# Performance work log

Measured on AMD Instinct MI355X. Metric: run time of the kernel, lower is better.

## Reference

```python
import jax, jax.numpy as jnp
import numpy as np

N, E, D_IN, D_OUT = 100000, 1600000, 64, 64


def setup_inputs() -> dict:
    key = jax.random.key(0)
    k0, k1, k2, k3 = jax.random.split(key, 4)
    x = jax.random.normal(k0, (N, D_IN), dtype=jnp.float32)
    edge_index = jax.random.randint(k1, (2, E), 0, N)  # [2, E] (src, dst)
    W = jax.random.normal(k2, (D_IN, D_OUT), dtype=jnp.float32) / np.sqrt(D_IN).astype(np.float32)
    b = jnp.zeros((D_OUT,), dtype=jnp.float32)
    causal_attention = jax.random.normal(k3, (D_OUT, D_OUT), dtype=jnp.float32)
    return {"x": x, "edge_index": edge_index, "W": W, "b": b,
            "causal_attention": causal_attention, "L": 1}


def gcn_conv(x, edge_index, W, b):
    # PyG GCNConv: x' = D^{-1/2} (A + I) D^{-1/2} (x W) + b
    n = x.shape[0]
    xw = x @ W  # [N, D_OUT]
    loops = jnp.arange(n)
    src = jnp.concatenate([edge_index[0], loops])  # [E+N]
    dst = jnp.concatenate([edge_index[1], loops])
    deg = jax.ops.segment_sum(jnp.ones_like(src, dtype=xw.dtype), dst, num_segments=n)
    dinv = jnp.where(deg > 0, jax.lax.rsqrt(deg), 0.0)
    norm = dinv[src] * dinv[dst]  # [E+N]
    agg = jax.ops.segment_sum(norm[:, None] * xw[src], dst, num_segments=n)  # [N, D_OUT]
    return agg + b


def reference(x, edge_index, W, b, causal_attention, L):
    x_conv = gcn_conv(x, edge_index, W, b)
    causal_weights = jax.nn.softmax(causal_attention, axis=1)  # row softmax
    return x_conv @ causal_weights  # [N, D_OUT]
```

## Files before the change

kernel.cpp:

```cpp
#include <hip/hip_runtime.h>
#include <hip/hip_bf16.h>


#define D 64
#define BSHIFT 7
#define BNODES 128
#define ARENA_CAP 3072
#define REBIN_CAP 8192
#define BIN_TILE 2048

__device__ __forceinline__ unsigned short f2bf(float f) {
    union { float f; unsigned int u; } c;
    c.f = f;
    unsigned int u = c.u;
    u += 0x7fffu + ((u >> 16) & 1u);
    return (unsigned short)(u >> 16);
}
__device__ __forceinline__ float bf2f(unsigned short r) {
    union { unsigned int u; float f; } c;
    c.u = ((unsigned int)r) << 16;
    return c.f;
}
__device__ __forceinline__ float bflo(unsigned int u) {
    union { unsigned int u; float f; } c;
    c.u = u << 16;
    return c.f;
}
__device__ __forceinline__ float bfhi(unsigned int u) {
    union { unsigned int u; float f; } c;
    c.u = u & 0xffff0000u;
    return c.f;
}

__global__ __launch_bounds__(256) void prep_kernel(const float* __restrict__ W,
                                                   const float* __restrict__ b,
                                                   const float* __restrict__ A,
                                                   float* __restrict__ M,
                                                   float* __restrict__ bs,
                                                   int* __restrict__ cursor, int nbuck) {
    __shared__ float S[D * D];
    int t = threadIdx.x;
    int gidx = blockIdx.x * 256 + t;
    if (gidx < nbuck) cursor[gidx] = gidx * ARENA_CAP;
    if (t < D) {
        float mx = -1e30f;
        for (int j = 0; j < D; j++) mx = fmaxf(mx, A[t * D + j]);
        float sum = 0.f;
        for (int j = 0; j < D; j++) {
            float v = __expf(A[t * D + j] - mx);
            S[t * D + j] = v;
            sum += v;
        }
        float inv = 1.f / sum;
        for (int j = 0; j < D; j++) S[t * D + j] *= inv;
    }
    __syncthreads();
    int k = blockIdx.x * 4 + (t >> 6);
    int j = t & 63;
    float acc = 0.f;
    for (int d = 0; d < D; d++) acc += W[k * D + d] * S[d * D + j];
    M[k * D + j] = acc;
    if (blockIdx.x == 0 && t < D) {
        float a2 = 0.f;
        for (int d = 0; d < D; d++) a2 += b[d] * S[d * D + t];
        bs[t] = a2;
    }
}

__global__ __launch_bounds__(256) void bin_kernel(const int* __restrict__ src,
                                                  const int* __restrict__ dst,
                                                  int* __restrict__ cursor,
                                                  int* __restrict__ binned, int E) {
    __shared__ int h[1024];
    __shared__ int pbuf[BIN_TILE];
    __shared__ unsigned short bb[BIN_TILE];
    int t = threadIdx.x;
    for (int i = t; i < 1024; i += 256) h[i] = 0;
    __syncthreads();
    int base = blockIdx.x * BIN_TILE;
    int cnt = min(E - base, BIN_TILE);
    for (int i = t; i < cnt; i += 256) {
        int s = src[base + i], d = dst[base + i];
        int bk = (d >> BSHIFT) & 1023;
        pbuf[i] = (s << BSHIFT) | (d & (BNODES - 1));
        bb[i] = (unsigned short)bk;
        atomicAdd(&h[bk], 1);
    }
    __syncthreads();
    for (int b = t; b < 1024; b += 256) {
        int c = h[b];
        if (c) h[b] = atomicAdd(&cursor[b], c);
    }
    __syncthreads();
    for (int i = t; i < cnt; i += 256) {
        int pos = atomicAdd(&h[bb[i]], 1);
        binned[pos] = pbuf[i];
    }
}

__global__ __launch_bounds__(256) void rebin_kernel(int* __restrict__ binned,
                                                    const int* __restrict__ cursor,
                                                    int* __restrict__ rowstart,
                                                    int* __restrict__ rowend,
                                                    float* __restrict__ dinv, int N) {
    __shared__ int buf[REBIN_CAP];
    __shared__ int h[BNODES];
    __shared__ int sc[BNODES];
    __shared__ int cur[BNODES];
    int t = threadIdx.x;
    int b = blockIdx.x;
    int s = b * ARENA_CAP;
    int cnt = cursor[b] - s;
    if (cnt > REBIN_CAP) cnt = REBIN_CAP;
    if (t < BNODES) h[t] = 0;
    __syncthreads();
    for (int i = t; i < cnt; i += 256) {
        int p = binned[s + i];
        buf[i] = p;
        atomicAdd(&h[p & (BNODES - 1)], 1);
    }
    __syncthreads();
    if (t < BNODES) sc[t] = h[t];
    __syncthreads();
    for (int off = 1; off < BNODES; off <<= 1) {
        int u = (t < BNODES && t >= off) ? sc[t - off] : 0;
        __syncthreads();
        if (t < BNODES) sc[t] += u;
        __syncthreads();
    }
    if (t < BNODES) {
        int ex = sc[t] - h[t];
        cur[t] = ex;
        int node = (b << BSHIFT) + t;
        if (node < N) {
            rowstart[node] = s + ex;
            rowend[node] = s + sc[t];
            dinv[node] = rsqrtf((float)(h[t] + 1));
        }
    }
    __syncthreads();
    for (int i = t; i < cnt; i += 256) {
        int p = buf[i];
        int pos = atomicAdd(&cur[p & (BNODES - 1)], 1);
        binned[s + pos] = (int)((unsigned)p >> BSHIFT);
    }
}

__global__ __launch_bounds__(256) void zmat_kernel(const float* __restrict__ x,
                                                   const float* __restrict__ M,
                                                   const float* __restrict__ dinv,
                                                   unsigned short* __restrict__ zbf, int n) {
    __shared__ float Ms[D * D];
    __shared__ float xs[16][D + 1];
    int t = threadIdx.x;
    for (int i = t; i < (D * D) / 4; i += 256)
        ((float4*)Ms)[i] = ((const float4*)M)[i];
    int row0 = blockIdx.x * 16;
    for (int i = t; i < 16 * D; i += 256) {
        int r = i >> 6, c = i & 63;
        xs[r][c] = (row0 + r < n) ? x[(size_t)(row0 + r) * D + c] : 0.f;
    }
    __syncthreads();
    int r = t >> 4;
    int jg = (t & 15) << 2;
    float4 acc = {0.f, 0.f, 0.f, 0.f};
#pragma unroll
    for (int k = 0; k < D; k++) {
        float xv = xs[r][k];
        float4 m = *(const float4*)&Ms[k * D + jg];
        acc.x += xv * m.x;
        acc.y += xv * m.y;
        acc.z += xv * m.z;
        acc.w += xv * m.w;
    }
    int row = row0 + r;
    if (row < n) {
        float di = dinv[row];
        ushort4 res;
        res.x = f2bf(di * acc.x);
        res.y = f2bf(di * acc.y);
        res.z = f2bf(di * acc.z);
        res.w = f2bf(di * acc.w);
        *(ushort4*)&zbf[(size_t)row * D + jg] = res;
    }
}

__global__ __launch_bounds__(256) void gather_kernel(const unsigned short* __restrict__ zbf,
                                                     const int* __restrict__ csr,
                                                     const int* __restrict__ rowstart,
                                                     const int* __restrict__ rowend,
                                                     const float* __restrict__ dinv,
                                                     const float* __restrict__ bs,
                                                     float* __restrict__ out, int n) {
    int node = blockIdx.x * 4 + (threadIdx.x >> 6);
    if (node >= n) return;
    int lane = threadIdx.x & 63;
    int g = lane >> 5;
    int c = lane & 31;
    int start = rowstart[node];
    int end = rowend[node];
    float a0 = 0.f, a1 = 0.f, a2 = 0.f, a3 = 0.f;
    int e = start;
    while (e < end) {
        int cnt = min(end - e, 64);
        int sreg = (lane < cnt) ? csr[e + lane] : 0;
        int k = 0;
        for (; k + 7 < cnt; k += 8) {
            int p0 = __shfl(sreg, k + g);
            int p1 = __shfl(sreg, k + 2 + g);
            int p2 = __shfl(sreg, k + 4 + g);
            int p3 = __shfl(sreg, k + 6 + g);
            unsigned u0 = *(const unsigned*)&zbf[(size_t)p0 * D + 2 * c];
            unsigned u1 = *(const unsigned*)&zbf[(size_t)p1 * D + 2 * c];
            unsigned u2 = *(const unsigned*)&zbf[(size_t)p2 * D + 2 * c];
            unsigned u3 = *(const unsigned*)&zbf[(size_t)p3 * D + 2 * c];
            a0 += bflo(u0); a1 += bfhi(u0);
            a2 += bflo(u1); a3 += bfhi(u1);
            a0 += bflo(u2); a1 += bfhi(u2);
            a2 += bflo(u3); a3 += bfhi(u3);
        }
        for (; k + 1 < cnt; k += 2) {
            int p = __shfl(sreg, k + g);
            unsigned u = *(const unsigned*)&zbf[(size_t)p * D + 2 * c];
            a0 += bflo(u); a1 += bfhi(u);
        }
        if (k < cnt) {
            int p = __shfl(sreg, k);
            unsigned u = *(const unsigned*)&zbf[(size_t)p * D + 2 * c];
            if (g == 0) { a0 += bflo(u); a1 += bfhi(u); }
        }
        e += cnt;
    }
    a0 += a2; a1 += a3;
    a0 += __shfl_xor(a0, 32);
    a1 += __shfl_xor(a1, 32);
    if (lane < 32) {
        unsigned uz = *(const unsigned*)&zbf[(size_t)node * D + 2 * c];
        float2 bb = ((const float2*)bs)[c];
        float di = dinv[node];
        float2 o;
        o.x = di * (a0 + bflo(uz)) + bb.x;
        o.y = di * (a1 + bfhi(uz)) + bb.y;
        ((float2*)&out[(size_t)node * D])[c] = o;
    }
}

extern "C" void kernel_launch(void* const* d_in, const int* in_sizes, int n_in,
                              void* d_out, int out_size, void* d_ws, size_t ws_size,
                              hipStream_t stream) {
    const float* x = (const float*)d_in[0];
    const int* ei = (const int*)d_in[1];
    const float* W = (const float*)d_in[2];
    const float* b = (const float*)d_in[3];
    const float* A = (const float*)d_in[4];

    const int N = in_sizes[0] / D;
    const int E = in_sizes[1] / 2;
    const int* src = ei;
    const int* dst = ei + E;
    const int NBUCK = (N + BNODES - 1) >> BSHIFT;

    char* ws = (char*)d_ws;
    size_t off = 0;
    auto alloc = [&](size_t bytes) -> char* {
        char* p = ws + off;
        off = (off + bytes + 255) & ~(size_t)255;
        return p;
    };
    int* cursor = (int*)alloc((size_t)NBUCK * 4);
    float* dinv = (float*)alloc((size_t)N * 4);
    float* M = (float*)alloc((size_t)D * D * 4);
    float* bs = (float*)alloc((size_t)D * 4);
    int* binned = (int*)alloc((size_t)NBUCK * ARENA_CAP * 4);
    int* rowstart = (int*)alloc((size_t)N * 4);
    int* rowend = (int*)alloc((size_t)N * 4);
    unsigned short* zbf = (unsigned short*)alloc((size_t)N * D * 2);
    (void)ws_size;

    prep_kernel<<<16, 256, 0, stream>>>(W, b, A, M, bs, cursor, NBUCK);
    bin_kernel<<<(E + BIN_TILE - 1) / BIN_TILE, 256, 0, stream>>>(src, dst, cursor, binned, E);
    rebin_kernel<<<NBUCK, 256, 0, stream>>>(binned, cursor, rowstart, rowend, dinv, N);
    zmat_kernel<<<(N + 15) / 16, 256, 0, stream>>>(x, M, dinv, zbf, N);
    gather_kernel<<<(N + 3) / 4, 256, 0, stream>>>(zbf, binned, rowstart, rowend, dinv, bs, (float*)d_out, N);
}
```

Before: 205.2 us.

## Fuse rebin and z-matrix kernels per bucket, enlarge bin tile

```diff
diff --git a/kernel.cpp b/kernel.cpp
--- a/kernel.cpp
+++ b/kernel.cpp
@@ -6,8 +6,7 @@
 #define BSHIFT 7
 #define BNODES 128
 #define ARENA_CAP 3072
-#define REBIN_CAP 8192
-#define BIN_TILE 2048
+#define BIN_TILE 8192
 
 __device__ __forceinline__ unsigned short f2bf(float f) {
     union { float f; unsigned int u; } c;
@@ -15,11 +14,6 @@
     unsigned int u = c.u;
     u += 0x7fffu + ((u >> 16) & 1u);
     return (unsigned short)(u >> 16);
-}
-__device__ __forceinline__ float bf2f(unsigned short r) {
-    union { unsigned int u; float f; } c;
-    c.u = ((unsigned int)r) << 16;
-    return c.f;
 }
 __device__ __forceinline__ float bflo(unsigned int u) {
     union { unsigned int u; float f; } c;
@@ -67,7 +61,7 @@
     }
 }
 
-__global__ __launch_bounds__(256) void bin_kernel(const int* __restrict__ src,
+__global__ __launch_bounds__(512) void bin_kernel(const int* __restrict__ src,
                                                   const int* __restrict__ dst,
                                                   int* __restrict__ cursor,
                                                   int* __restrict__ binned, int E) {
@@ -75,11 +69,11 @@
     __shared__ int pbuf[BIN_TILE];
     __shared__ unsigned short bb[BIN_TILE];
     int t = threadIdx.x;
-    for (int i = t; i < 1024; i += 256) h[i] = 0;
+    for (int i = t; i < 1024; i += 512) h[i] = 0;
     __syncthreads();
     int base = blockIdx.x * BIN_TILE;
     int cnt = min(E - base, BIN_TILE);
-    for (int i = t; i < cnt; i += 256) {
+    for (int i = t; i < cnt; i += 512) {
         int s = src[base + i], d = dst[base + i];
         int bk = (d >> BSHIFT) & 1023;
         pbuf[i] = (s << BSHIFT) | (d & (BNODES - 1));
@@ -87,23 +81,30 @@
         atomicAdd(&h[bk], 1);
     }
     __syncthreads();
-    for (int b = t; b < 1024; b += 256) {
+    for (int b = t; b < 1024; b += 512) {
         int c = h[b];
         if (c) h[b] = atomicAdd(&cursor[b], c);
     }
     __syncthreads();
-    for (int i = t; i < cnt; i += 256) {
+    for (int i = t; i < cnt; i += 512) {
         int pos = atomicAdd(&h[bb[i]], 1);
         binned[pos] = pbuf[i];
     }
 }
 
-__global__ __launch_bounds__(256) void rebin_kernel(int* __restrict__ binned,
-                                                    const int* __restrict__ cursor,
-                                                    int* __restrict__ rowstart,
-                                                    int* __restrict__ rowend,
-                                                    float* __restrict__ dinv, int N) {
-    __shared__ int buf[REBIN_CAP];
+__global__ __launch_bounds__(256) void rebin_zmat_kernel(const float* __restrict__ x,
+                                                         const float* __restrict__ M,
+                                                         int* __restrict__ binned,
+                                                         const int* __restrict__ cursor,
+                                                         int* __restrict__ rowstart,
+                                                         int* __restrict__ rowend,
+                                                         float* __restrict__ dinv,
+                                                         unsigned short* __restrict__ zbf,
+                                                         int N) {
+    __shared__ int buf[ARENA_CAP];
+    __shared__ float Ms[D * D];
+    __shared__ float xs[16][D + 1];
+    __shared__ float dv[BNODES];
     __shared__ int h[BNODES];
     __shared__ int sc[BNODES];
     __shared__ int cur[BNODES];
@@ -111,7 +112,9 @@
     int b = blockIdx.x;
     int s = b * ARENA_CAP;
     int cnt = cursor[b] - s;
-    if (cnt > REBIN_CAP) cnt = REBIN_CAP;
+    if (cnt > ARENA_CAP) cnt = ARENA_CAP;
+    for (int i = t; i < (D * D) / 4; i += 256)
+        ((float4*)Ms)[i] = ((const float4*)M)[i];
     if (t < BNODES) h[t] = 0;
     __syncthreads();
     for (int i = t; i < cnt; i += 256) {
@@ -131,11 +134,13 @@
     if (t < BNODES) {
         int ex = sc[t] - h[t];
         cur[t] = ex;
+        float di = rsqrtf((float)(h[t] + 1));
+        dv[t] = di;
         int node = (b << BSHIFT) + t;
         if (node < N) {
             rowstart[node] = s + ex;
             rowend[node] = s + sc[t];
-            dinv[node] = rsqrtf((float)(h[t] + 1));
+            dinv[node] = di;
         }
     }
     __syncthreads();
@@ -144,44 +149,36 @@
         int pos = atomicAdd(&cur[p & (BNODES - 1)], 1);
         binned[s + pos] = (int)((unsigned)p >> BSHIFT);
     }
-}
-
-__global__ __launch_bounds__(256) void zmat_kernel(const float* __restrict__ x,
-                                                   const float* __restrict__ M,
-                                                   const float* __restrict__ dinv,
-                                                   unsigned short* __restrict__ zbf, int n) {
-    __shared__ float Ms[D * D];
-    __shared__ float xs[16][D + 1];
-    int t = threadIdx.x;
-    for (int i = t; i < (D * D) / 4; i += 256)
-        ((float4*)Ms)[i] = ((const float4*)M)[i];
-    int row0 = blockIdx.x * 16;
-    for (int i = t; i < 16 * D; i += 256) {
-        int r = i >> 6, c = i & 63;
-        xs[r][c] = (row0 + r < n) ? x[(size_t)(row0 + r) * D + c] : 0.f;
-    }
-    __syncthreads();
-    int r = t >> 4;
-    int jg = (t & 15) << 2;
-    float4 acc = {0.f, 0.f, 0.f, 0.f};
+    for (int rc = 0; rc < 8; rc++) {
+        __syncthreads();
+        int row0 = (b << BSHIFT) + rc * 16;
+        for (int i = t; i < 16 * D; i += 256) {
+            int r = i >> 6, c = i & 63;
+            xs[r][c] = (row0 + r < N) ? x[(size_t)(row0 + r) * D + c] : 0.f;
+        }
+        __syncthreads();
+        int r = t >> 4;
+        int jg = (t & 15) << 2;
+        float4 acc = {0.f, 0.f, 0.f, 0.f};
 #pragma unroll
-    for (int k = 0; k < D; k++) {
-        float xv = xs[r][k];
-        float4 m = *(const float4*)&Ms[k * D + jg];
-        acc.x += xv * m.x;
-        acc.y += xv * m.y;
-        acc.z += xv * m.z;
-        acc.w += xv * m.w;
-    }
-    int row = row0 + r;
-    if (row < n) {
-        float di = dinv[row];
-        ushort4 res;
-        res.x = f2bf(di * acc.x);
-        res.y = f2bf(di * acc.y);
-        res.z = f2bf(di * acc.z);
-        res.w = f2bf(di * acc.w);
-        *(ushort4*)&zbf[(size_t)row * D + jg] = res;
+        for (int k = 0; k < D; k++) {
+            float xv = xs[r][k];
+            float4 m = *(const float4*)&Ms[k * D + jg];
+            acc.x += xv * m.x;
+            acc.y += xv * m.y;
+            acc.z += xv * m.z;
+            acc.w += xv * m.w;
+        }
+        int row = row0 + r;
+        if (row < N) {
+            float di = dv[rc * 16 + r];
+            ushort4 res;
+            res.x = f2bf(di * acc.x);
+            res.y = f2bf(di * acc.y);
+            res.z = f2bf(di * acc.z);
+            res.w = f2bf(di * acc.w);
+            *(ushort4*)&zbf[(size_t)row * D + jg] = res;
+        }
     }
 }
 
@@ -278,8 +275,7 @@
     (void)ws_size;
 
     prep_kernel<<<16, 256, 0, stream>>>(W, b, A, M, bs, cursor, NBUCK);
-    bin_kernel<<<(E + BIN_TILE - 1) / BIN_TILE, 256, 0, stream>>>(src, dst, cursor, binned, E);
-    rebin_kernel<<<NBUCK, 256, 0, stream>>>(binned, cursor, rowstart, rowend, dinv, N);
-    zmat_kernel<<<(N + 15) / 16, 256, 0, stream>>>(x, M, dinv, zbf, N);
+    bin_kernel<<<(E + BIN_TILE - 1) / BIN_TILE, 512, 0, stream>>>(src, dst, cursor, binned, E);
+    rebin_zmat_kernel<<<NBUCK, 256, 0, stream>>>(x, M, binned, cursor, rowstart, rowend, dinv, zbf, N);
     gather_kernel<<<(N + 3) / 4, 256, 0, stream>>>(zbf, binned, rowstart, rowend, dinv, bs, (float*)d_out, N);
 }
```

Result: faster. 198.3 us (-3.4%).
